# Performance work log

Hardware: AMD Instinct MI355X
Metric: run time of the kernel (lower is better)

## Reference

```python
import jax, jax.numpy as jnp
import numpy as np

HEADS = 8
EPS = 1e-5


def setup_inputs() -> dict:
    key = jax.random.key(0)
    ks = jax.random.split(key, 4)
    B, S, N, C = 1, 192, 256, 256
    msa = jax.random.normal(ks[0], (B, S, N, C), dtype=jnp.float32)
    w_qkv = jax.random.normal(ks[1], (3 * C, C), dtype=jnp.float32) * 0.02
    b_qkv = jnp.zeros((3 * C,), dtype=jnp.float32)
    w_out = jax.random.normal(ks[2], (C, C), dtype=jnp.float32) * 0.02
    b_out = jnp.zeros((C,), dtype=jnp.float32)
    gamma = jnp.ones((C,), dtype=jnp.float32)
    beta = jnp.zeros((C,), dtype=jnp.float32)
    return {"msa": msa, "w_qkv": w_qkv, "b_qkv": b_qkv, "w_out": w_out,
            "b_out": b_out, "gamma": gamma, "beta": beta}


def reference(msa, w_qkv, b_qkv, w_out, b_out, gamma, beta):
    B, S, N, C = msa.shape
    H = HEADS
    D = C // H
    scale = D ** -0.5
    # column attention: attend over the S (MSA depth) axis per residue n
    msa_t = jnp.transpose(msa, (0, 2, 1, 3))                 # [B,N,S,C]
    qkv = msa_t @ w_qkv.T + b_qkv                             # [B,N,S,3C]
    qkv = qkv.reshape(B, N, S, 3, H, D)
    q, k, v = qkv[..., 0, :, :], qkv[..., 1, :, :], qkv[..., 2, :, :]  # [B,N,S,H,D]
    attn = jnp.einsum('bnshd,bnthd->bnhst', q, k) * scale     # [B,N,H,S,S]
    attn = jax.nn.softmax(attn, axis=-1)
    out = jnp.einsum('bnhst,bnthd->bnshd', attn, v).reshape(B, N, S, C)
    out = jnp.transpose(out, (0, 2, 1, 3))                    # [B,S,N,C]
    out = out @ w_out.T + b_out
    x = msa + out
    mu = jnp.mean(x, axis=-1, keepdims=True)
    var = jnp.mean(jnp.square(x - mu), axis=-1, keepdims=True)
    return (x - mu) * jax.lax.rsqrt(var + EPS) * gamma + beta
```

## Files before the change

### kernel.cpp

```cpp
#include <hip/hip_runtime.h>
#include <stdint.h>

#define S_DIM 192
#define N_DIM 256
#define C_DIM 256
#define H_DIM 8
#define D_DIM 32
#define QKV_STRIDE (N_DIM * H_DIM * S_DIM * D_DIM)

typedef float f32x4 __attribute__((ext_vector_type(4)));
typedef float f32x16 __attribute__((ext_vector_type(16)));
typedef short bf16x8 __attribute__((ext_vector_type(8)));

__device__ __forceinline__ unsigned short f2bf(float f) {
  union { float f; unsigned u; } v; v.f = f;
  unsigned r = v.u + 0x7FFFu + ((v.u >> 16) & 1u);
  return (unsigned short)(r >> 16);
}

__device__ __forceinline__ unsigned cvt_pk_bf16(float lo, float hi) {
  unsigned r;
  asm("v_cvt_pk_bf16_f32 %0, %1, %2" : "=v"(r) : "v"(lo), "v"(hi));
  return r;
}

__device__ __forceinline__ void gl2lds16(const void* g, void* l) {
  __builtin_amdgcn_global_load_lds(
      (const __attribute__((address_space(1))) unsigned int*)g,
      (__attribute__((address_space(3))) unsigned int*)l, 16, 0, 0);
}

__global__ __launch_bounds__(256) void k_prep(const float* __restrict__ msa,
                                              unsigned short* __restrict__ A,
                                              const float* __restrict__ wq,
                                              const float* __restrict__ wo,
                                              unsigned short* __restrict__ dq,
                                              unsigned short* __restrict__ do_) {
  int b = blockIdx.x;
  if (b < 12288) {
    int tid = b * 256 + threadIdx.x;
    int token = tid >> 6;
    int c4 = tid & 63;
    int n = token / S_DIM;
    int s = token - n * S_DIM;
    float4 v = *(const float4*)(msa + ((size_t)(s * N_DIM + n) << 8) + (c4 << 2));
    ushort4 o;
    o.x = f2bf(v.x); o.y = f2bf(v.y); o.z = f2bf(v.z); o.w = f2bf(v.w);
    *(ushort4*)(A + ((size_t)token << 8) + (c4 << 2)) = o;
  } else {
    int tid = (b - 12288) * 256 + threadIdx.x;
    const float* src; unsigned short* dst; int idx;
    if (tid < 49152) { src = wq; dst = dq; idx = tid; }
    else { src = wo; dst = do_; idx = tid - 49152; }
    float4 v = *(const float4*)(src + (size_t)idx * 4);
    ushort4 o;
    o.x = f2bf(v.x); o.y = f2bf(v.y); o.z = f2bf(v.z); o.w = f2bf(v.w);
    *(ushort4*)(dst + (size_t)idx * 4) = o;
  }
}

__global__ __launch_bounds__(256) void k_qkv(const unsigned short* __restrict__ A,
                                             const unsigned short* __restrict__ W,
                                             const float* __restrict__ bq,
                                             unsigned short* __restrict__ qkv) {
  __shared__ unsigned short As[128 * 64];
  __shared__ unsigned short Bs[128 * 64];
  const int tid = threadIdx.x;
  const int lane = tid & 63, wid = tid >> 6;
  const int l16 = lane & 15, lg = lane >> 4;
  const int wr = wid >> 1, wc = wid & 1;
  const int p = blockIdx.x;
  const int o = (p & 7) * 288 + (p >> 3);
  const int bm0 = (o / 6) * 128;
  const int bn0 = (o % 6) * 128;
  const int lrow = lane >> 3, lchunk = lane & 7;
  const int sw = ((lchunk ^ lrow) * 8);

  f32x4 acc[4][4] = {};

  for (int ks = 0; ks < 4; ks++) {
    const int k0 = ks * 64;
    __syncthreads();
#pragma unroll
    for (int q = 0; q < 4; q++) {
      int base_row = wid * 32 + q * 8;
      gl2lds16(A + (size_t)(bm0 + base_row + lrow) * 256 + k0 + sw, &As[base_row * 64]);
    }
#pragma unroll
    for (int q = 0; q < 4; q++) {
      int base_row = wid * 32 + q * 8;
      gl2lds16(W + (size_t)(bn0 + base_row + lrow) * 256 + k0 + sw, &Bs[base_row * 64]);
    }
    __syncthreads();
#pragma unroll
    for (int kk = 0; kk < 2; kk++) {
      const int xr = ((kk * 4 + lg) ^ (l16 & 7)) * 8;
      bf16x8 a[4], b[4];
#pragma unroll
      for (int m = 0; m < 4; m++)
        a[m] = *(const bf16x8*)&As[(wr * 64 + m * 16 + l16) * 64 + xr];
#pragma unroll
      for (int n2 = 0; n2 < 4; n2++)
        b[n2] = *(const bf16x8*)&Bs[(wc * 64 + n2 * 16 + l16) * 64 + xr];
      if (bn0 < 512) {
#pragma unroll
        for (int m = 0; m < 4; m++)
#pragma unroll
          for (int n2 = 0; n2 < 4; n2++)
            acc[m][n2] = __builtin_amdgcn_mfma_f32_16x16x32_bf16(b[n2], a[m], acc[m][n2], 0, 0, 0);
      } else {
#pragma unroll
        for (int m = 0; m < 4; m++)
#pragma unroll
          for (int n2 = 0; n2 < 4; n2++)
            acc[m][n2] = __builtin_amdgcn_mfma_f32_16x16x32_bf16(a[m], b[n2], acc[m][n2], 0, 0, 0);
      }
    }
  }

  const int t3 = bn0 >> 8;
  if (t3 < 2) {
#pragma unroll
    for (int n2 = 0; n2 < 4; n2++) {
      int j0 = bn0 + wc * 64 + n2 * 16 + lg * 4;
      float4 b4 = *(const float4*)&bq[j0];
      int c0 = j0 & 255;
      int h = c0 >> 5, d0 = c0 & 31;
#pragma unroll
      for (int m = 0; m < 4; m++) {
        int token = bm0 + wr * 64 + m * 16 + l16;
        int n = token / S_DIM;
        int s = token - n * S_DIM;
        ushort4 o2;
        o2.x = f2bf(acc[m][n2][0] + b4.x);
        o2.y = f2bf(acc[m][n2][1] + b4.y);
        o2.z = f2bf(acc[m][n2][2] + b4.z);
        o2.w = f2bf(acc[m][n2][3] + b4.w);
        *(ushort4*)(qkv + (size_t)t3 * QKV_STRIDE +
                    ((size_t)((n * 8 + h) * 192 + s)) * 32 + d0) = o2;
      }
    }
  } else {
#pragma unroll
    for (int n2 = 0; n2 < 4; n2++) {
      int j = bn0 + wc * 64 + n2 * 16 + l16;
      int hd = j - 512;
      int h = hd >> 5, d = hd & 31;
      float bias = bq[j];
#pragma unroll
      for (int m = 0; m < 4; m++) {
        int t0 = bm0 + wr * 64 + m * 16 + lg * 4;
        int n = t0 / S_DIM;
        int s0 = t0 - n * S_DIM;
        ushort4 o2;
        o2.x = f2bf(acc[m][n2][0] + bias);
        o2.y = f2bf(acc[m][n2][1] + bias);
        o2.z = f2bf(acc[m][n2][2] + bias);
        o2.w = f2bf(acc[m][n2][3] + bias);
        *(ushort4*)(qkv + (size_t)2 * QKV_STRIDE + ((size_t)(n * 8 + h) * 32 + d) * 192 + s0) = o2;
      }
    }
  }
}

__global__ __launch_bounds__(384) void k_attn2(const unsigned short* __restrict__ qkv,
                                               unsigned short* __restrict__ attn_out) {
  const int lane = threadIdx.x & 63;
  const int l32 = lane & 31;
  const int hi = lane >> 5;
  const int qt = threadIdx.x >> 6;
  const int nh = blockIdx.x;
  const int n = nh >> 3, h = nh & 7;
  const unsigned short* Qp = qkv + (size_t)nh * (192 * 32);
  const unsigned short* Kp = qkv + (size_t)QKV_STRIDE + (size_t)nh * (192 * 32);
  const unsigned short* Vt = qkv + (size_t)2 * QKV_STRIDE + (size_t)nh * (32 * 192);
  const int q0 = qt * 32;

  bf16x8 bq0 = *(const bf16x8*)(Qp + (q0 + l32) * 32 + hi * 8);
  bf16x8 bq1 = *(const bf16x8*)(Qp + (q0 + l32) * 32 + 16 + hi * 8);

  f32x16 accO = {};
  float m_run = -1e30f, l_run = 0.f;
  const float scale = 0.17677669529663687f;
  const float DEFER = 8.0f / 0.17677669529663687f;

  bf16x8 ka0 = *(const bf16x8*)(Kp + l32 * 32 + hi * 8);
  bf16x8 ka1 = *(const bf16x8*)(Kp + l32 * 32 + 16 + hi * 8);
  bf16x8 va0 = *(const bf16x8*)(Vt + (size_t)l32 * 192 + hi * 8);
  bf16x8 va1 = *(const bf16x8*)(Vt + (size_t)l32 * 192 + 16 + hi * 8);

#pragma unroll
  for (int t = 0; t < 6; t++) {
    bf16x8 kn0, kn1, vn0, vn1;
    if (t < 5) {
      kn0 = *(const bf16x8*)(Kp + ((t + 1) * 32 + l32) * 32 + hi * 8);
      kn1 = *(const bf16x8*)(Kp + ((t + 1) * 32 + l32) * 32 + 16 + hi * 8);
      vn0 = *(const bf16x8*)(Vt + (size_t)l32 * 192 + (t + 1) * 32 + hi * 8);
      vn1 = *(const bf16x8*)(Vt + (size_t)l32 * 192 + (t + 1) * 32 + 16 + hi * 8);
    }
    f32x16 sv = {};
    sv = __builtin_amdgcn_mfma_f32_32x32x16_bf16(ka0, bq0, sv, 0, 0, 0);
    sv = __builtin_amdgcn_mfma_f32_32x32x16_bf16(ka1, bq1, sv, 0, 0, 0);

    float tmx = sv[0];
#pragma unroll
    for (int r = 1; r < 16; r++) tmx = fmaxf(tmx, sv[r]);
    tmx = fmaxf(tmx, __shfl_xor(tmx, 32));

    bool need = tmx > m_run + DEFER;
    if (__ballot(need)) {
      float m_new = fmaxf(m_run, tmx);
      float corr = __expf((m_run - m_new) * scale);
      l_run *= corr;
#pragma unroll
      for (int r = 0; r < 16; r++) {
        int qr = (r & 3) + 8 * (r >> 2) + 4 * hi;
        accO[r] *= __shfl(corr, qr);
      }
      m_run = m_new;
    }

    float ssum = 0.f;
#pragma unroll
    for (int r = 0; r < 16; r++) {
      float p2 = __expf((sv[r] - m_run) * scale);
      sv[r] = p2;
      ssum += p2;
    }
    ssum += __shfl_xor(ssum, 32);
    l_run += ssum;

    unsigned pk[8];
#pragma unroll
    for (int g = 0; g < 4; g++) {
      pk[2 * g]     = cvt_pk_bf16(sv[4 * g],     sv[4 * g + 1]);
      pk[2 * g + 1] = cvt_pk_bf16(sv[4 * g + 2], sv[4 * g + 3]);
    }

#pragma unroll
    for (int kh = 0; kh < 2; kh++) {
      unsigned sa = hi ? pk[4 * kh]     : pk[4 * kh + 2];
      unsigned sb = hi ? pk[4 * kh + 1] : pk[4 * kh + 3];
      unsigned pa = __shfl_xor((int)sa, 32);
      unsigned pb = __shfl_xor((int)sb, 32);
      union { unsigned u[4]; bf16x8 v; } af;
      af.u[0] = hi ? pa : pk[4 * kh];
      af.u[1] = hi ? pb : pk[4 * kh + 1];
      af.u[2] = hi ? pk[4 * kh + 2] : pa;
      af.u[3] = hi ? pk[4 * kh + 3] : pb;
      accO = __builtin_amdgcn_mfma_f32_32x32x16_bf16(af.v, kh ? va1 : va0, accO, 0, 0, 0);
    }
    ka0 = kn0; ka1 = kn1; va0 = vn0; va1 = vn1;
  }

  float inv = 1.0f / l_run;
#pragma unroll
  for (int r = 0; r < 16; r++) {
    int qr = (r & 3) + 8 * (r >> 2) + 4 * hi;
    float v = accO[r] * __shfl(inv, qr);
    attn_out[((size_t)((q0 + qr) * 256 + n)) * 256 + h * 32 + l32] = f2bf(v);
  }
}

__global__ __launch_bounds__(256) void k_out(const unsigned short* __restrict__ Aat,
                                             const unsigned short* __restrict__ W,
                                             const float* __restrict__ bo,
                                             const float* __restrict__ msa,
                                             const float* __restrict__ gamma,
                                             const float* __restrict__ beta,
                                             float* __restrict__ out) {
  __shared__ unsigned short As[64 * 64];
  __shared__ unsigned short Bs[256 * 64];
  const int tid = threadIdx.x;
  const int lane = tid & 63, wid = tid >> 6;
  const int l16 = lane & 15, lg = lane >> 4;
  const int bm0 = blockIdx.x * 64;
  const int lrow = lane >> 3, lchunk = lane & 7;
  const int sw = ((lchunk ^ lrow) * 8);

  f32x4 acc[16] = {};

  for (int ks = 0; ks < 4; ks++) {
    const int k0 = ks * 64;
    __syncthreads();
#pragma unroll
    for (int q = 0; q < 2; q++) {
      int base_row = q * 32 + wid * 8;
      gl2lds16(Aat + (size_t)(bm0 + base_row + lrow) * 256 + k0 + sw, &As[base_row * 64]);
    }
#pragma unroll
    for (int q = 0; q < 8; q++) {
      int base_row = wid * 64 + q * 8;
      gl2lds16(W + (size_t)(base_row + lrow) * 256 + k0 + sw, &Bs[base_row * 64]);
    }
    __syncthreads();
#pragma unroll
    for (int kk = 0; kk < 2; kk++) {
      const int xr = ((kk * 4 + lg) ^ (l16 & 7)) * 8;
      bf16x8 a = *(const bf16x8*)&As[(wid * 16 + l16) * 64 + xr];
#pragma unroll
      for (int c = 0; c < 16; c++) {
        bf16x8 b = *(const bf16x8*)&Bs[(c * 16 + l16) * 64 + xr];
        acc[c] = __builtin_amdgcn_mfma_f32_16x16x32_bf16(a, b, acc[c], 0, 0, 0);
      }
    }
  }

#pragma unroll
  for (int c = 0; c < 16; c++) {
    int col = c * 16 + l16;
    float bias = bo[col];
#pragma unroll
    for (int i = 0; i < 4; i++) {
      int row = bm0 + wid * 16 + lg * 4 + i;
      acc[c][i] += bias + msa[(size_t)row * 256 + col];
    }
  }
#pragma unroll
  for (int i = 0; i < 4; i++) {
    float s1 = 0.f, s2 = 0.f;
#pragma unroll
    for (int c = 0; c < 16; c++) { float x = acc[c][i]; s1 += x; s2 += x * x; }
    s1 += __shfl_xor(s1, 1); s2 += __shfl_xor(s2, 1);
    s1 += __shfl_xor(s1, 2); s2 += __shfl_xor(s2, 2);
    s1 += __shfl_xor(s1, 4); s2 += __shfl_xor(s2, 4);
    s1 += __shfl_xor(s1, 8); s2 += __shfl_xor(s2, 8);
    float mu = s1 * (1.0f / 256.0f);
    float var = s2 * (1.0f / 256.0f) - mu * mu;
    float rstd = rsqrtf(var + 1e-5f);
    int row = bm0 + wid * 16 + lg * 4 + i;
#pragma unroll
    for (int c = 0; c < 16; c++) {
      int col = c * 16 + l16;
      float y = (acc[c][i] - mu) * rstd * gamma[col] + beta[col];
      out[(size_t)row * 256 + col] = y;
    }
  }
}

extern "C" void kernel_launch(void* const* d_in, const int* in_sizes, int n_in,
                              void* d_out, int out_size, void* d_ws, size_t ws_size,
                              hipStream_t stream) {
  const float* msa   = (const float*)d_in[0];
  const float* w_qkv = (const float*)d_in[1];
  const float* b_qkv = (const float*)d_in[2];
  const float* w_out = (const float*)d_in[3];
  const float* b_out = (const float*)d_in[4];
  const float* gamma = (const float*)d_in[5];
  const float* beta  = (const float*)d_in[6];
  float* out = (float*)d_out;

  char* ws = (char*)d_ws;
  unsigned short* A      = (unsigned short*)(ws);
  unsigned short* qkvbuf = (unsigned short*)(ws + 25165824ull);
  unsigned short* wq_bf  = (unsigned short*)(ws + 4ull * 25165824ull);
  unsigned short* wo_bf  = (unsigned short*)(ws + 4ull * 25165824ull + 393216ull);

  k_prep<<<12544, 256, 0, stream>>>(msa, A, w_qkv, w_out, wq_bf, wo_bf);
  k_qkv<<<2304, 256, 0, stream>>>(A, wq_bf, b_qkv, qkvbuf);
  k_attn2<<<2048, 384, 0, stream>>>(qkvbuf, A);
  k_out<<<768, 256, 0, stream>>>(A, wo_bf, b_out, msa, gamma, beta, out);
}
```

Baseline: 122.6 us.

## Fuse msa transpose and bf16 conversion into QKV GEMM tile loads

Drops the separate prep pass that transposed msa and wrote a bf16 copy. The QKV GEMM now loads fp32 msa rows directly into LDS with the column gather and an XOR swizzle, then converts to bf16 with v_cvt_pk_bf16 when it reads the operands. This saves a full write and re-read of the intermediate activation, but the A tile in LDS doubles in size and each tile load reads twice the bytes. Every GEMM column block also re-converts the same rows.

```diff
diff --git a/kernel.cpp b/kernel.cpp
--- a/kernel.cpp
+++ b/kernel.cpp
@@ -30,40 +30,25 @@
       (__attribute__((address_space(3))) unsigned int*)l, 16, 0, 0);
 }
 
-__global__ __launch_bounds__(256) void k_prep(const float* __restrict__ msa,
-                                              unsigned short* __restrict__ A,
-                                              const float* __restrict__ wq,
+__global__ __launch_bounds__(256) void k_cvt2(const float* __restrict__ wq,
                                               const float* __restrict__ wo,
                                               unsigned short* __restrict__ dq,
                                               unsigned short* __restrict__ do_) {
-  int b = blockIdx.x;
-  if (b < 12288) {
-    int tid = b * 256 + threadIdx.x;
-    int token = tid >> 6;
-    int c4 = tid & 63;
-    int n = token / S_DIM;
-    int s = token - n * S_DIM;
-    float4 v = *(const float4*)(msa + ((size_t)(s * N_DIM + n) << 8) + (c4 << 2));
-    ushort4 o;
-    o.x = f2bf(v.x); o.y = f2bf(v.y); o.z = f2bf(v.z); o.w = f2bf(v.w);
-    *(ushort4*)(A + ((size_t)token << 8) + (c4 << 2)) = o;
-  } else {
-    int tid = (b - 12288) * 256 + threadIdx.x;
-    const float* src; unsigned short* dst; int idx;
-    if (tid < 49152) { src = wq; dst = dq; idx = tid; }
-    else { src = wo; dst = do_; idx = tid - 49152; }
-    float4 v = *(const float4*)(src + (size_t)idx * 4);
-    ushort4 o;
-    o.x = f2bf(v.x); o.y = f2bf(v.y); o.z = f2bf(v.z); o.w = f2bf(v.w);
-    *(ushort4*)(dst + (size_t)idx * 4) = o;
-  }
-}
-
-__global__ __launch_bounds__(256) void k_qkv(const unsigned short* __restrict__ A,
+  int tid = blockIdx.x * 256 + threadIdx.x;
+  const float* src; unsigned short* dst; int idx;
+  if (tid < 49152) { src = wq; dst = dq; idx = tid; }
+  else { src = wo; dst = do_; idx = tid - 49152; }
+  float4 v = *(const float4*)(src + (size_t)idx * 4);
+  ushort4 o;
+  o.x = f2bf(v.x); o.y = f2bf(v.y); o.z = f2bf(v.z); o.w = f2bf(v.w);
+  *(ushort4*)(dst + (size_t)idx * 4) = o;
+}
+
+__global__ __launch_bounds__(256) void k_qkv(const float* __restrict__ msa,
                                              const unsigned short* __restrict__ W,
                                              const float* __restrict__ bq,
                                              unsigned short* __restrict__ qkv) {
-  __shared__ unsigned short As[128 * 64];
+  __shared__ float Asf[128 * 64];
   __shared__ unsigned short Bs[128 * 64];
   const int tid = threadIdx.x;
   const int lane = tid & 63, wid = tid >> 6;
@@ -82,9 +67,15 @@
     const int k0 = ks * 64;
     __syncthreads();
 #pragma unroll
-    for (int q = 0; q < 4; q++) {
-      int base_row = wid * 32 + q * 8;
-      gl2lds16(A + (size_t)(bm0 + base_row + lrow) * 256 + k0 + sw, &As[base_row * 64]);
+    for (int q = 0; q < 8; q++) {
+      int base_row = wid * 32 + q * 4;
+      int row = base_row + (lane >> 4);
+      int token = bm0 + row;
+      int nn = token / S_DIM;
+      int ss = token - nn * S_DIM;
+      int lc = (lane & 15) ^ (row & 15);
+      gl2lds16(msa + (size_t)(ss * 256 + nn) * 256 + k0 + lc * 4,
+               &Asf[base_row * 64]);
     }
 #pragma unroll
     for (int q = 0; q < 4; q++) {
@@ -97,8 +88,19 @@
       const int xr = ((kk * 4 + lg) ^ (l16 & 7)) * 8;
       bf16x8 a[4], b[4];
 #pragma unroll
-      for (int m = 0; m < 4; m++)
-        a[m] = *(const bf16x8*)&As[(wr * 64 + m * 16 + l16) * 64 + xr];
+      for (int m = 0; m < 4; m++) {
+        int R = wr * 64 + m * 16 + l16;
+        int p1 = (2 * (kk * 4 + lg)) ^ l16;
+        int p2 = p1 ^ 1;
+        f32x4 d0 = *(const f32x4*)((const char*)Asf + R * 256 + p1 * 16);
+        f32x4 d1 = *(const f32x4*)((const char*)Asf + R * 256 + p2 * 16);
+        union { unsigned u[4]; bf16x8 v; } t;
+        t.u[0] = cvt_pk_bf16(d0[0], d0[1]);
+        t.u[1] = cvt_pk_bf16(d0[2], d0[3]);
+        t.u[2] = cvt_pk_bf16(d1[0], d1[1]);
+        t.u[3] = cvt_pk_bf16(d1[2], d1[3]);
+        a[m] = t.v;
+      }
 #pragma unroll
       for (int n2 = 0; n2 < 4; n2++)
         b[n2] = *(const bf16x8*)&Bs[(wc * 64 + n2 * 16 + l16) * 64 + xr];
@@ -351,13 +353,13 @@
   float* out = (float*)d_out;
 
   char* ws = (char*)d_ws;
-  unsigned short* A      = (unsigned short*)(ws);
-  unsigned short* qkvbuf = (unsigned short*)(ws + 25165824ull);
-  unsigned short* wq_bf  = (unsigned short*)(ws + 4ull * 25165824ull);
-  unsigned short* wo_bf  = (unsigned short*)(ws + 4ull * 25165824ull + 393216ull);
-
-  k_prep<<<12544, 256, 0, stream>>>(msa, A, w_qkv, w_out, wq_bf, wo_bf);
-  k_qkv<<<2304, 256, 0, stream>>>(A, wq_bf, b_qkv, qkvbuf);
-  k_attn2<<<2048, 384, 0, stream>>>(qkvbuf, A);
-  k_out<<<768, 256, 0, stream>>>(A, wo_bf, b_out, msa, gamma, beta, out);
-}
+  unsigned short* qkvbuf = (unsigned short*)(ws);
+  unsigned short* attn   = (unsigned short*)(ws + 75497472ull);
+  unsigned short* wq_bf  = (unsigned short*)(ws + 75497472ull + 25165824ull);
+  unsigned short* wo_bf  = (unsigned short*)(ws + 75497472ull + 25165824ull + 393216ull);
+
+  k_cvt2<<<256, 256, 0, stream>>>(w_qkv, w_out, wq_bf, wo_bf);
+  k_qkv<<<2304, 256, 0, stream>>>(msa, wq_bf, b_qkv, qkvbuf);
+  k_attn2<<<2048, 384, 0, stream>>>(qkvbuf, attn);
+  k_out<<<768, 256, 0, stream>>>(attn, wo_bf, b_out, msa, gamma, beta, out);
+}
```

Result: no change. 122.4 us, median of 2 (-0.2%).
